# Optimization experiments

Hardware: AMD Instinct MI355X
Metric: run time of the kernel (lower is better)

Reference implementation:

```python
import jax, jax.numpy as jnp
import numpy as np

B, N, C, H = 8, 1024, 768, 12
D = C // H  # 64


def setup_inputs() -> dict:
    key = jax.random.key(0)
    ks = jax.random.split(key, 6)
    x = jax.random.normal(ks[0], (B, N, C), dtype=jnp.float32)
    pad_mask = jnp.ones((B, N), dtype=jnp.int32)
    # params (torch Linear stored transposed; here kept as (in, out) for x @ W)
    s = 1.0 / np.sqrt(C)
    w_attn = jax.random.uniform(ks[1], (C, 3 * C), jnp.float32, -s, s)
    b_attn = jax.random.uniform(ks[2], (3 * C,), jnp.float32, -s, s)
    w_proj = jax.random.uniform(ks[3], (C, C), jnp.float32, -s, s)
    b_proj = jax.random.uniform(ks[4], (C,), jnp.float32, -s, s)
    return {"x": x, "pad_mask": pad_mask, "w_attn": w_attn,
            "b_attn": b_attn, "w_proj": w_proj, "b_proj": b_proj}


def reference(x, pad_mask, w_attn, b_attn, w_proj, b_proj):
    # qkv projection
    qkv = x @ w_attn + b_attn                      # [B,N,3C]
    q, k, v = jnp.split(qkv, 3, axis=-1)
    q = q.reshape(B, N, H, D).transpose(0, 2, 1, 3)  # [B,H,N,D]
    k = k.reshape(B, N, H, D).transpose(0, 2, 1, 3)
    v = v.reshape(B, N, H, D).transpose(0, 2, 1, 3)
    scale = 1.0 / np.sqrt(D)
    att = jnp.einsum('bhqd,bhkd->bhqk', q, k) * scale  # [B,H,N,N]
    # NOTE: original code's causal masked_fill is non-in-place and discarded,
    # so the causal mask is NOT applied. Only the pad mask (over query rows) is.
    pm = pad_mask.reshape(B, 1, N, 1)
    att = jnp.where(pm == 0, -jnp.inf, att)
    att = jax.nn.softmax(att, axis=-1)
    out = jnp.einsum('bhqk,bhkd->bhqd', att, v)     # [B,H,N,D]
    out = out.transpose(0, 2, 1, 3).reshape(B, N, C)
    # dropout layers are identity in eval mode
    return out @ w_proj + b_proj
```

## Files before the change

### kernel.cpp

```cpp
#include <hip/hip_runtime.h>
#include <hip/hip_bf16.h>

#define B_  8
#define N_  1024
#define C_  768
#define H_  12
#define D_  64
#define C3  2304
#define C2  1536

typedef unsigned short ushort_t;
typedef __attribute__((ext_vector_type(8))) short bf16x8;
typedef __attribute__((ext_vector_type(4))) float f32x4;

__device__ __forceinline__ float bf2f(ushort_t u) {
    union { unsigned int i; float f; } v;
    v.i = ((unsigned int)u) << 16;
    return v.f;
}

__device__ __forceinline__ ushort_t f2bf(float f) {
    union { float f; unsigned int i; } v;
    v.f = f;
    unsigned int x = v.i;
    if ((x & 0x7f800000u) == 0x7f800000u && (x & 0x007fffffu))
        return (ushort_t)((x >> 16) | 0x0040u);
    return (ushort_t)((x + 0x7fffu + ((x >> 16) & 1u)) >> 16);
}

__device__ __forceinline__ void st1(float* p, float v) { *p = v; }
__device__ __forceinline__ void st1(ushort_t* p, float v) { *p = f2bf(v); }

__global__ __launch_bounds__(256) void cvt_bf16(
    const float* __restrict__ X, ushort_t* __restrict__ Y, int n)
{
    int i = (blockIdx.x * 256 + threadIdx.x) * 4;
    if (i < n) {
        float4 f = *reinterpret_cast<const float4*>(X + i);
        ushort4 o;
        o.x = f2bf(f.x); o.y = f2bf(f.y); o.z = f2bf(f.z); o.w = f2bf(f.w);
        *reinterpret_cast<ushort4*>(Y + i) = o;
    }
}

__global__ __launch_bounds__(256) void transpose_to_bf16(
    const float* __restrict__ W, ushort_t* __restrict__ WT, int K, int Nn)
{
    __shared__ float t[32][33];
    const int n0 = blockIdx.x * 32, k0 = blockIdx.y * 32;
    const int tx = threadIdx.x & 31, ty = threadIdx.x >> 5;
    #pragma unroll
    for (int i = 0; i < 4; ++i) {
        const int k = ty + i * 8;
        t[k][tx] = W[(size_t)(k0 + k) * Nn + n0 + tx];
    }
    __syncthreads();
    #pragma unroll
    for (int i = 0; i < 4; ++i) {
        const int n = ty + i * 8;
        WT[(size_t)(n0 + n) * K + k0 + tx] = f2bf(t[tx][n]);
    }
}

#define GBK 64

__device__ __forceinline__ void gld_lds16(const ushort_t* g, ushort_t* lds) {
    __builtin_amdgcn_global_load_lds(
        (const __attribute__((address_space(1))) void*)g,
        (__attribute__((address_space(3))) void*)lds, 16, 0, 0);
}

template<typename TO, bool SCALEQ>
__global__ __launch_bounds__(256) void gemm_mfma(
    const ushort_t* __restrict__ A, const ushort_t* __restrict__ BT,
    const float* __restrict__ bias, TO* __restrict__ Y, int ldY,
    ushort_t* __restrict__ vtOut, int M, int K, int Nn)
{
    __shared__ ushort_t As[128 * GBK];
    __shared__ ushort_t Bs[128 * GBK];

    const int tid  = threadIdx.x;
    const int wave = tid >> 6;
    const int lane = tid & 63;
    const int row0 = blockIdx.y * 128;
    const int col0 = blockIdx.x * 128;
    const int wr   = (wave >> 1) * 64;
    const int wc   = (wave & 1) * 64;
    const int l15  = lane & 15;
    const int quad = lane >> 4;
    const int l7   = l15 & 7;

    const int srow = lane >> 3;
    const int sg   = (lane & 7) ^ srow;

    f32x4 acc[4][4] = {};

    for (int k0 = 0; k0 < K; k0 += GBK) {
        __syncthreads();
        #pragma unroll
        for (int it = 0; it < 4; ++it) {
            const int baseRow = wave * 32 + it * 8;
            const int r = baseRow + srow;
            gld_lds16(&A [(size_t)(row0 + r) * K + k0 + sg * 8], &As[baseRow * GBK]);
            gld_lds16(&BT[(size_t)(col0 + r) * K + k0 + sg * 8], &Bs[baseRow * GBK]);
        }
        __syncthreads();

        #pragma unroll
        for (int kc = 0; kc < 2; ++kc) {
            bf16x8 af[4], bf[4];
            #pragma unroll
            for (int i = 0; i < 4; ++i) {
                const int aslot = (kc * 4 + quad) ^ l7;
                af[i] = *reinterpret_cast<const bf16x8*>(
                    &As[(wr + i * 16 + l15) * GBK + aslot * 8]);
                bf[i] = *reinterpret_cast<const bf16x8*>(
                    &Bs[(wc + i * 16 + l15) * GBK + aslot * 8]);
            }
            #pragma unroll
            for (int i = 0; i < 4; ++i)
                #pragma unroll
                for (int j = 0; j < 4; ++j)
                    acc[i][j] = __builtin_amdgcn_mfma_f32_16x16x32_bf16(
                        af[i], bf[j], acc[i][j], 0, 0, 0);
        }
    }

    const float qs = (SCALEQ && (col0 + wc) < C_) ? 0.125f : 1.0f;

    if (vtOut != nullptr && col0 >= C2) {
        #pragma unroll
        for (int i = 0; i < 4; ++i) {
            const int r0 = row0 + wr + i * 16 + quad * 4;
            const int bb = r0 >> 10;
            const int n  = r0 & 1023;
            #pragma unroll
            for (int j = 0; j < 4; ++j) {
                const int c  = col0 + wc + j * 16 + l15;
                const int cv = c - C2;
                const int hh = cv >> 6, d = cv & 63;
                const float bv = bias[c];
                ushort4 o;
                o.x = f2bf(acc[i][j][0] + bv);
                o.y = f2bf(acc[i][j][1] + bv);
                o.z = f2bf(acc[i][j][2] + bv);
                o.w = f2bf(acc[i][j][3] + bv);
                *reinterpret_cast<ushort4*>(
                    &vtOut[((size_t)(bb * H_ + hh) * D_ + d) * N_ + n]) = o;
            }
        }
    } else {
        #pragma unroll
        for (int i = 0; i < 4; ++i) {
            const int r = row0 + wr + i * 16 + quad * 4;
            #pragma unroll
            for (int j = 0; j < 4; ++j) {
                const int c = col0 + wc + j * 16 + l15;
                const float bv = bias[c];
                #pragma unroll
                for (int t = 0; t < 4; ++t)
                    st1(&Y[(size_t)(r + t) * ldY + c], (acc[i][j][t] + bv) * qs);
            }
        }
    }
}

#define LDT 72

__global__ __launch_bounds__(256) void attn_mfma(
    const ushort_t* __restrict__ qk, const ushort_t* __restrict__ vt,
    const int* __restrict__ pad_mask, ushort_t* __restrict__ y)
{
    __shared__ ushort_t Ks [64 * LDT];
    __shared__ ushort_t Vts[64 * LDT];
    __shared__ ushort_t Ps [4][32 * LDT];

    const int tid  = threadIdx.x;
    const int wave = tid >> 6;
    const int lane = tid & 63;
    const int l15  = lane & 15;
    const int quad = lane >> 4;

    const int qt = blockIdx.x & 7;
    const int h  = (blockIdx.x >> 3) % H_;
    const int b  = blockIdx.x / (8 * H_);
    const int q0 = qt * 128 + wave * 32;

    const ushort_t* qkB = qk + (size_t)b * N_ * C2;
    const ushort_t* vtB = vt + ((size_t)(b * H_ + h)) * D_ * N_;
    const int ho = h * D_;

    bf16x8 qf[2][2];
    #pragma unroll
    for (int rt = 0; rt < 2; ++rt)
        #pragma unroll
        for (int kc = 0; kc < 2; ++kc)
            qf[rt][kc] = *reinterpret_cast<const bf16x8*>(
                &qkB[(size_t)(q0 + rt * 16 + l15) * C2 + ho + kc * 32 + quad * 8]);

    int mrow[2][4];
    #pragma unroll
    for (int rt = 0; rt < 2; ++rt)
        #pragma unroll
        for (int t = 0; t < 4; ++t)
            mrow[rt][t] = pad_mask[b * N_ + q0 + rt * 16 + quad * 4 + t];

    f32x4 oacc[2][4] = {};
    float den[2][4] = {};

    const int srow = tid >> 3;
    const int scol = (tid & 7) * 8;

    for (int k0 = 0; k0 < N_; k0 += 64) {
        __syncthreads();
        #pragma unroll
        for (int half = 0; half < 2; ++half) {
            const int r = srow + half * 32;
            uint4 kv = *reinterpret_cast<const uint4*>(
                &qkB[(size_t)(k0 + r) * C2 + C_ + ho + scol]);
            uint4 vv = *reinterpret_cast<const uint4*>(
                &vtB[(size_t)r * N_ + k0 + scol]);
            *reinterpret_cast<uint4*>(&Ks [r * LDT + scol]) = kv;
            *reinterpret_cast<uint4*>(&Vts[r * LDT + scol]) = vv;
        }
        __syncthreads();

        f32x4 s[2][4] = {};
        #pragma unroll
        for (int kc = 0; kc < 2; ++kc) {
            bf16x8 kf[4];
            #pragma unroll
            for (int ct = 0; ct < 4; ++ct)
                kf[ct] = *reinterpret_cast<const bf16x8*>(
                    &Ks[(ct * 16 + l15) * LDT + kc * 32 + quad * 8]);
            #pragma unroll
            for (int rt = 0; rt < 2; ++rt)
                #pragma unroll
                for (int ct = 0; ct < 4; ++ct)
                    s[rt][ct] = __builtin_amdgcn_mfma_f32_16x16x32_bf16(
                        qf[rt][kc], kf[ct], s[rt][ct], 0, 0, 0);
        }

        ushort_t* Pw = Ps[wave];
        #pragma unroll
        for (int rt = 0; rt < 2; ++rt)
            #pragma unroll
            for (int ct = 0; ct < 4; ++ct)
                #pragma unroll
                for (int t = 0; t < 4; ++t) {
                    float p = __expf(s[rt][ct][t]);
                    unsigned u = (__float_as_uint(p) + 0x8000u) & 0xffff0000u;
                    den[rt][t] += __uint_as_float(u);
                    Pw[(rt * 16 + quad * 4 + t) * LDT + ct * 16 + l15] =
                        (ushort_t)(u >> 16);
                }

        #pragma unroll
        for (int kc = 0; kc < 2; ++kc) {
            bf16x8 pf[2], vf[4];
            #pragma unroll
            for (int rt = 0; rt < 2; ++rt)
                pf[rt] = *reinterpret_cast<const bf16x8*>(
                    &Pw[(rt * 16 + l15) * LDT + kc * 32 + quad * 8]);
            #pragma unroll
            for (int dt = 0; dt < 4; ++dt)
                vf[dt] = *reinterpret_cast<const bf16x8*>(
                    &Vts[(dt * 16 + l15) * LDT + kc * 32 + quad * 8]);
            #pragma unroll
            for (int rt = 0; rt < 2; ++rt)
                #pragma unroll
                for (int dt = 0; dt < 4; ++dt)
                    oacc[rt][dt] = __builtin_amdgcn_mfma_f32_16x16x32_bf16(
                        pf[rt], vf[dt], oacc[rt][dt], 0, 0, 0);
        }
    }

    ushort_t* Pw = Ps[wave];
    #pragma unroll
    for (int rt = 0; rt < 2; ++rt)
        #pragma unroll
        for (int t = 0; t < 4; ++t) {
            float v = den[rt][t];
            v += __shfl_xor(v, 1);
            v += __shfl_xor(v, 2);
            v += __shfl_xor(v, 4);
            v += __shfl_xor(v, 8);
            const float inv = mrow[rt][t] ? 1.0f / v : __builtin_nanf("");
            const int row = rt * 16 + quad * 4 + t;
            #pragma unroll
            for (int dt = 0; dt < 4; ++dt)
                Pw[row * LDT + dt * 16 + l15] = f2bf(oacc[rt][dt][t] * inv);
        }
    {
        const int orow = lane >> 1;
        const int ocol = (lane & 1) * 32;
        const size_t gr = (size_t)(b * N_ + q0 + orow) * C_ + ho + ocol;
        #pragma unroll
        for (int i2 = 0; i2 < 4; ++i2) {
            uint4 w = *reinterpret_cast<const uint4*>(&Pw[orow * LDT + ocol + i2 * 8]);
            *reinterpret_cast<uint4*>(&y[gr + i2 * 8]) = w;
        }
    }
}

extern "C" void kernel_launch(void* const* d_in, const int* in_sizes, int n_in,
                              void* d_out, int out_size, void* d_ws, size_t ws_size,
                              hipStream_t stream)
{
    const float* x      = (const float*)d_in[0];
    const int*   pad    = (const int*)d_in[1];
    const float* w_attn = (const float*)d_in[2];
    const float* b_attn = (const float*)d_in[3];
    const float* w_proj = (const float*)d_in[4];
    const float* b_proj = (const float*)d_in[5];
    float* out = (float*)d_out;

    ushort_t* qkb = (ushort_t*)d_ws;
    ushort_t* vtb = qkb + (size_t)B_ * N_ * C2;
    ushort_t* y   = vtb + (size_t)B_ * H_ * D_ * N_;
    ushort_t* xb  = y;
    ushort_t* wat = y + (size_t)B_ * N_ * C_;
    ushort_t* wpt = wat + (size_t)C3 * C_;

    const int M = B_ * N_;

    cvt_bf16<<<dim3((M * C_) / (256 * 4)), dim3(256), 0, stream>>>(x, xb, M * C_);
    transpose_to_bf16<<<dim3(C3 / 32, C_ / 32), dim3(256), 0, stream>>>(
        w_attn, wat, C_, C3);
    transpose_to_bf16<<<dim3(C_ / 32, C_ / 32), dim3(256), 0, stream>>>(
        w_proj, wpt, C_, C_);

    gemm_mfma<ushort_t, true><<<dim3(C3 / 128, M / 128), dim3(256), 0, stream>>>(
        xb, wat, b_attn, qkb, C2, vtb, M, C_, C3);

    attn_mfma<<<dim3(B_ * H_ * 8), dim3(256), 0, stream>>>(qkb, vtb, pad, y);

    gemm_mfma<float, false><<<dim3(C_ / 128, M / 128), dim3(256), 0, stream>>>(
        y, wpt, b_proj, out, C_, nullptr, M, C_, C_);
}
```

Before: 219.1 us.

## Keep attention probabilities in registers via transposed MFMA and double-buffer K/V tiles

The attention kernel now computes S transposed (K as the A operand), so each lane's exp'd scores map directly onto the B operand of a 16x16x16 bf16 MFMA for the PV product. This removes the per-wave LDS round trip for P and the LDS staging of the output. K/V tiles are double-buffered, with the next tile's global loads issued before compute and stored to LDS afterward, which removes one barrier per iteration. The softmax uses exp2 with log2(e) folded into the Q scale, and the denominator now sums unrounded probabilities instead of the bf16-rounded values used in the numerator.

```diff
diff --git a/kernel.cpp b/kernel.cpp
--- a/kernel.cpp
+++ b/kernel.cpp
@@ -11,7 +11,22 @@
 
 typedef unsigned short ushort_t;
 typedef __attribute__((ext_vector_type(8))) short bf16x8;
+typedef __attribute__((ext_vector_type(4))) short bf16x4;
 typedef __attribute__((ext_vector_type(4))) float f32x4;
+
+#if __has_builtin(__builtin_amdgcn_mfma_f32_16x16x16_bf16)
+#define MFMA16(A, B, C) __builtin_amdgcn_mfma_f32_16x16x16_bf16(A, B, C, 0, 0, 0)
+#else
+#define MFMA16(A, B, C) __builtin_amdgcn_mfma_f32_16x16x16bf16_1k(A, B, C, 0, 0, 0)
+#endif
+
+__device__ __forceinline__ float fast_exp2(float x) {
+#if __has_builtin(__builtin_amdgcn_exp2f)
+    return __builtin_amdgcn_exp2f(x);
+#else
+    return exp2f(x);
+#endif
+}
 
 __device__ __forceinline__ float bf2f(ushort_t u) {
     union { unsigned int i; float f; } v;
@@ -63,6 +78,7 @@
 }
 
 #define GBK 64
+#define QSCALE 0.18033688011112042f
 
 __device__ __forceinline__ void gld_lds16(const ushort_t* g, ushort_t* lds) {
     __builtin_amdgcn_global_load_lds(
@@ -126,7 +142,7 @@
         }
     }
 
-    const float qs = (SCALEQ && (col0 + wc) < C_) ? 0.125f : 1.0f;
+    const float qs = (SCALEQ && (col0 + wc) < C_) ? QSCALE : 1.0f;
 
     if (vtOut != nullptr && col0 >= C2) {
         #pragma unroll
@@ -171,9 +187,8 @@
     const ushort_t* __restrict__ qk, const ushort_t* __restrict__ vt,
     const int* __restrict__ pad_mask, ushort_t* __restrict__ y)
 {
-    __shared__ ushort_t Ks [64 * LDT];
-    __shared__ ushort_t Vts[64 * LDT];
-    __shared__ ushort_t Ps [4][32 * LDT];
+    __shared__ ushort_t Ks [2][64 * LDT];
+    __shared__ ushort_t Vts[2][64 * LDT];
 
     const int tid  = threadIdx.x;
     const int wave = tid >> 6;
@@ -198,30 +213,43 @@
             qf[rt][kc] = *reinterpret_cast<const bf16x8*>(
                 &qkB[(size_t)(q0 + rt * 16 + l15) * C2 + ho + kc * 32 + quad * 8]);
 
-    int mrow[2][4];
+    int mrow[2];
     #pragma unroll
     for (int rt = 0; rt < 2; ++rt)
-        #pragma unroll
-        for (int t = 0; t < 4; ++t)
-            mrow[rt][t] = pad_mask[b * N_ + q0 + rt * 16 + quad * 4 + t];
+        mrow[rt] = pad_mask[b * N_ + q0 + rt * 16 + l15];
 
     f32x4 oacc[2][4] = {};
-    float den[2][4] = {};
+    float den[2] = {};
 
     const int srow = tid >> 3;
     const int scol = (tid & 7) * 8;
 
-    for (int k0 = 0; k0 < N_; k0 += 64) {
-        __syncthreads();
-        #pragma unroll
-        for (int half = 0; half < 2; ++half) {
-            const int r = srow + half * 32;
-            uint4 kv = *reinterpret_cast<const uint4*>(
-                &qkB[(size_t)(k0 + r) * C2 + C_ + ho + scol]);
-            uint4 vv = *reinterpret_cast<const uint4*>(
-                &vtB[(size_t)r * N_ + k0 + scol]);
-            *reinterpret_cast<uint4*>(&Ks [r * LDT + scol]) = kv;
-            *reinterpret_cast<uint4*>(&Vts[r * LDT + scol]) = vv;
+    uint4 kr[2], vr[2];
+    #pragma unroll
+    for (int half = 0; half < 2; ++half) {
+        const int r = srow + half * 32;
+        kr[half] = *reinterpret_cast<const uint4*>(&qkB[(size_t)r * C2 + C_ + ho + scol]);
+        vr[half] = *reinterpret_cast<const uint4*>(&vtB[(size_t)r * N_ + scol]);
+    }
+    #pragma unroll
+    for (int half = 0; half < 2; ++half) {
+        const int r = srow + half * 32;
+        *reinterpret_cast<uint4*>(&Ks [0][r * LDT + scol]) = kr[half];
+        *reinterpret_cast<uint4*>(&Vts[0][r * LDT + scol]) = vr[half];
+    }
+
+    for (int kt = 0; kt < 16; ++kt) {
+        const int cur = kt & 1;
+        if (kt < 15) {
+            const int k0 = (kt + 1) * 64;
+            #pragma unroll
+            for (int half = 0; half < 2; ++half) {
+                const int r = srow + half * 32;
+                kr[half] = *reinterpret_cast<const uint4*>(
+                    &qkB[(size_t)(k0 + r) * C2 + C_ + ho + scol]);
+                vr[half] = *reinterpret_cast<const uint4*>(
+                    &vtB[(size_t)r * N_ + k0 + scol]);
+            }
         }
         __syncthreads();
 
@@ -232,73 +260,73 @@
             #pragma unroll
             for (int ct = 0; ct < 4; ++ct)
                 kf[ct] = *reinterpret_cast<const bf16x8*>(
-                    &Ks[(ct * 16 + l15) * LDT + kc * 32 + quad * 8]);
+                    &Ks[cur][(ct * 16 + l15) * LDT + kc * 32 + quad * 8]);
             #pragma unroll
             for (int rt = 0; rt < 2; ++rt)
                 #pragma unroll
                 for (int ct = 0; ct < 4; ++ct)
                     s[rt][ct] = __builtin_amdgcn_mfma_f32_16x16x32_bf16(
-                        qf[rt][kc], kf[ct], s[rt][ct], 0, 0, 0);
-        }
-
-        ushort_t* Pw = Ps[wave];
+                        kf[ct], qf[rt][kc], s[rt][ct], 0, 0, 0);
+        }
+
+        bf16x4 pb[2][4];
         #pragma unroll
         for (int rt = 0; rt < 2; ++rt)
             #pragma unroll
-            for (int ct = 0; ct < 4; ++ct)
-                #pragma unroll
-                for (int t = 0; t < 4; ++t) {
-                    float p = __expf(s[rt][ct][t]);
-                    unsigned u = (__float_as_uint(p) + 0x8000u) & 0xffff0000u;
-                    den[rt][t] += __uint_as_float(u);
-                    Pw[(rt * 16 + quad * 4 + t) * LDT + ct * 16 + l15] =
-                        (ushort_t)(u >> 16);
-                }
-
-        #pragma unroll
-        for (int kc = 0; kc < 2; ++kc) {
-            bf16x8 pf[2], vf[4];
-            #pragma unroll
-            for (int rt = 0; rt < 2; ++rt)
-                pf[rt] = *reinterpret_cast<const bf16x8*>(
-                    &Pw[(rt * 16 + l15) * LDT + kc * 32 + quad * 8]);
+            for (int ct = 0; ct < 4; ++ct) {
+                float p0 = fast_exp2(s[rt][ct][0]);
+                float p1 = fast_exp2(s[rt][ct][1]);
+                float p2 = fast_exp2(s[rt][ct][2]);
+                float p3 = fast_exp2(s[rt][ct][3]);
+                den[rt] += (p0 + p1) + (p2 + p3);
+                union { unsigned u[2]; bf16x4 v; } pk;
+                pk.u[0] = ((__float_as_uint(p0) + 0x8000u) >> 16)
+                        | ((__float_as_uint(p1) + 0x8000u) & 0xffff0000u);
+                pk.u[1] = ((__float_as_uint(p2) + 0x8000u) >> 16)
+                        | ((__float_as_uint(p3) + 0x8000u) & 0xffff0000u);
+                pb[rt][ct] = pk.v;
+            }
+
+        #pragma unroll
+        for (int kk = 0; kk < 4; ++kk) {
+            bf16x4 va[4];
             #pragma unroll
             for (int dt = 0; dt < 4; ++dt)
-                vf[dt] = *reinterpret_cast<const bf16x8*>(
-                    &Vts[(dt * 16 + l15) * LDT + kc * 32 + quad * 8]);
+                va[dt] = *reinterpret_cast<const bf16x4*>(
+                    &Vts[cur][(dt * 16 + l15) * LDT + kk * 16 + quad * 4]);
             #pragma unroll
             for (int rt = 0; rt < 2; ++rt)
                 #pragma unroll
                 for (int dt = 0; dt < 4; ++dt)
-                    oacc[rt][dt] = __builtin_amdgcn_mfma_f32_16x16x32_bf16(
-                        pf[rt], vf[dt], oacc[rt][dt], 0, 0, 0);
-        }
-    }
-
-    ushort_t* Pw = Ps[wave];
-    #pragma unroll
-    for (int rt = 0; rt < 2; ++rt)
-        #pragma unroll
-        for (int t = 0; t < 4; ++t) {
-            float v = den[rt][t];
-            v += __shfl_xor(v, 1);
-            v += __shfl_xor(v, 2);
-            v += __shfl_xor(v, 4);
-            v += __shfl_xor(v, 8);
-            const float inv = mrow[rt][t] ? 1.0f / v : __builtin_nanf("");
-            const int row = rt * 16 + quad * 4 + t;
-            #pragma unroll
-            for (int dt = 0; dt < 4; ++dt)
-                Pw[row * LDT + dt * 16 + l15] = f2bf(oacc[rt][dt][t] * inv);
-        }
-    {
-        const int orow = lane >> 1;
-        const int ocol = (lane & 1) * 32;
-        const size_t gr = (size_t)(b * N_ + q0 + orow) * C_ + ho + ocol;
-        #pragma unroll
-        for (int i2 = 0; i2 < 4; ++i2) {
-            uint4 w = *reinterpret_cast<const uint4*>(&Pw[orow * LDT + ocol + i2 * 8]);
-            *reinterpret_cast<uint4*>(&y[gr + i2 * 8]) = w;
+                    oacc[rt][dt] = MFMA16(va[dt], pb[rt][kk], oacc[rt][dt]);
+        }
+
+        if (kt < 15) {
+            #pragma unroll
+            for (int half = 0; half < 2; ++half) {
+                const int r = srow + half * 32;
+                *reinterpret_cast<uint4*>(&Ks [cur ^ 1][r * LDT + scol]) = kr[half];
+                *reinterpret_cast<uint4*>(&Vts[cur ^ 1][r * LDT + scol]) = vr[half];
+            }
+        }
+    }
+
+    #pragma unroll
+    for (int rt = 0; rt < 2; ++rt) {
+        float v = den[rt];
+        v += __shfl_xor(v, 16);
+        v += __shfl_xor(v, 32);
+        const float inv = mrow[rt] ? 1.0f / v : __builtin_nanf("");
+        const size_t row = (size_t)(b * N_ + q0 + rt * 16 + l15);
+        #pragma unroll
+        for (int dt = 0; dt < 4; ++dt) {
+            ushort4 o;
+            o.x = f2bf(oacc[rt][dt][0] * inv);
+            o.y = f2bf(oacc[rt][dt][1] * inv);
+            o.z = f2bf(oacc[rt][dt][2] * inv);
+            o.w = f2bf(oacc[rt][dt][3] * inv);
+            *reinterpret_cast<ushort4*>(
+                &y[row * C_ + ho + dt * 16 + quad * 4]) = o;
         }
     }
 }
```

Result: slower. 239.8 us (+9.4%).
